# Kernel tuning notes

Hardware: AMD Instinct MI355X
Metric: run time of the kernel (lower is better)

The kernel has to match this reference:

```python
import jax, jax.numpy as jnp
import numpy as np

B, N, C, H = 16, 1024, 768, 12
D = C // H          # head dim = 64
HID = 4 * C         # 3072
EPS = 1e-5


def layernorm(x, g, b):
    m = x.mean(-1, keepdims=True)
    v = ((x - m) ** 2).mean(-1, keepdims=True)
    return (x - m) * jax.lax.rsqrt(v + EPS) * g + b


def setup_inputs() -> dict:
    key = jax.random.key(0)
    ks = jax.random.split(key, 10)
    s = 0.02
    return {
        "x": jax.random.normal(ks[0], (B, N, C), dtype=jnp.float32),
        "ln1_g": jnp.ones((C,), jnp.float32), "ln1_b": jnp.zeros((C,), jnp.float32),
        "wq": jax.random.normal(ks[1], (C, C)) * s, "bq": jnp.zeros((C,), jnp.float32),
        "wk": jax.random.normal(ks[2], (C, C)) * s, "bk": jnp.zeros((C,), jnp.float32),
        "wv": jax.random.normal(ks[3], (C, C)) * s, "bv": jnp.zeros((C,), jnp.float32),
        "wp": jax.random.normal(ks[4], (C, C)) * s, "bp": jnp.zeros((C,), jnp.float32),
        "ln2_g": jnp.ones((C,), jnp.float32), "ln2_b": jnp.zeros((C,), jnp.float32),
        "w1": jax.random.normal(ks[5], (HID, C)) * s, "b1": jnp.zeros((HID,), jnp.float32),
        "w2": jax.random.normal(ks[6], (C, HID)) * s, "b2": jnp.zeros((C,), jnp.float32),
        "gate_h": jax.random.normal(ks[7], (H,), dtype=jnp.float32),
        "gate_f": jax.random.normal(ks[8], (HID,), dtype=jnp.float32),
    }


def reference(x, ln1_g, ln1_b, wq, bq, wk, bk, wv, bv, wp, bp,
              ln2_g, ln2_b, w1, b1, w2, b2, gate_h, gate_f):
    # steady-state path: k_dynamic=None, is_warmup=False -> dyn gates are all ones,
    # so head_mask / ffn_mask reduce to the hard static gates (STE is identity on ones).
    head_mask = (jax.nn.sigmoid(gate_h) > 0.5).astype(x.dtype)            # [H]
    hm = jnp.broadcast_to(head_mask, (B, H))                              # [B,H]

    # --- attention branch ---
    xn = layernorm(x, ln1_g, ln1_b)
    split = lambda t: t.reshape(B, N, H, D).transpose(0, 2, 1, 3)          # [B,H,N,D]
    q = split(xn @ wq.T + bq)
    k = split(xn @ wk.T + bk)
    v = split(xn @ wv.T + bv)
    scale = D ** -0.5
    attn = jax.nn.softmax(jnp.einsum('bhqd,bhkd->bhqk', q, k) * scale, axis=-1)
    y = jnp.einsum('bhqk,bhkd->bhqd', attn, v)
    y = y * hm[:, :, None, None]                                           # per-head mask on y
    xa = y.transpose(0, 2, 1, 3).reshape(B, N, C)
    hm_flat = jnp.repeat(hm, D, axis=-1).reshape(B, 1, C)                  # mask applied a 2nd time
    xa = (xa * hm_flat) @ wp.T + bp
    x = x + xa

    # --- gated MLP branch ---
    fmask = (jax.nn.sigmoid(gate_f) > 0.5).astype(x.dtype)[None, None, :]  # [1,1,HID]
    xn2 = layernorm(x, ln2_g, ln2_b)
    f1 = xn2 @ w1.T + b1
    f1 = jax.nn.gelu(f1 * fmask, approximate=False) * fmask                # mask -> GELU -> mask
    x = x + f1 @ w2.T + b2
    return x
```

## Files before the change

kernel.cpp:

```cpp
#include <hip/hip_runtime.h>

#define BB 16
#define NNN 1024
#define CC 768
#define HH 12
#define DD 64
#define HIDN 3072
#define ROWS (BB*NNN)

typedef _Float16 half8 __attribute__((ext_vector_type(8)));
typedef _Float16 half4 __attribute__((ext_vector_type(4)));
typedef float floatx4 __attribute__((ext_vector_type(4)));

#define GLOAD_LDS(g, l) __builtin_amdgcn_global_load_lds( \
    (const __attribute__((address_space(1))) void*)(g),    \
    (__attribute__((address_space(3))) void*)(l), 16, 0, 0)

#define RAW_BARRIER() do { asm volatile("" ::: "memory"); \
    __builtin_amdgcn_s_barrier(); asm volatile("" ::: "memory"); } while (0)
#define VMCNT_WAIT(n) __builtin_amdgcn_s_waitcnt((n) | 0x0F70)

__global__ void cvt_kernel(const float* __restrict__ src, _Float16* __restrict__ dst, int n4) {
    int i = blockIdx.x * blockDim.x + threadIdx.x;
    if (i < n4) {
        floatx4 v = ((const floatx4*)src)[i];
        half4 h;
        h[0] = (_Float16)v[0]; h[1] = (_Float16)v[1];
        h[2] = (_Float16)v[2]; h[3] = (_Float16)v[3];
        ((half4*)dst)[i] = h;
    }
}

__global__ __launch_bounds__(256) void scan_kernel(const float* __restrict__ gf,
                                                   const float* __restrict__ b1,
                                                   int* __restrict__ meta,
                                                   int* __restrict__ perm,
                                                   float* __restrict__ b1c) {
    int t = threadIdx.x;
    int base = t * 12;
    bool act[12];
    int cnt = 0;
    #pragma unroll
    for (int i = 0; i < 12; i++) { bool a = gf[base + i] > 0.0f; act[i] = a; cnt += a ? 1 : 0; }
    __shared__ int cs[256];
    cs[t] = cnt;
    __syncthreads();
    if (t == 0) {
        int s = 0;
        for (int i = 0; i < 256; i++) { int c = cs[i]; cs[i] = s; s += c; }
        meta[1] = s;
        meta[0] = (s + 127) & ~127;
    }
    __syncthreads();
    int off = cs[t];
    for (int i = t; i < HIDN; i += 256) { b1c[i] = 0.0f; perm[i] = -1; }
    __syncthreads();
    #pragma unroll
    for (int i = 0; i < 12; i++)
        if (act[i]) { perm[off] = base + i; b1c[off] = b1[base + i]; off++; }
}

__global__ void gatherW1_kernel(const float* __restrict__ src, const int* __restrict__ perm,
                                _Float16* __restrict__ dst) {
    int i = blockIdx.x * blockDim.x + threadIdx.x;
    int row = i / 192, c4 = i - row * 192;
    int s = perm[row];
    half4 h; h[0] = h[1] = h[2] = h[3] = (_Float16)0.0f;
    if (s >= 0) {
        floatx4 v = ((const floatx4*)(src + (size_t)s * CC))[c4];
        h[0] = (_Float16)v[0]; h[1] = (_Float16)v[1];
        h[2] = (_Float16)v[2]; h[3] = (_Float16)v[3];
    }
    ((half4*)dst)[i] = h;
}

__global__ void gatherW2_kernel(const float* __restrict__ src, const int* __restrict__ perm,
                                _Float16* __restrict__ dst) {
    int i = blockIdx.x * blockDim.x + threadIdx.x;
    int n = i / 768, j4 = (i - n * 768) * 4;
    const float* r = src + (size_t)n * HIDN;
    half4 h;
    #pragma unroll
    for (int e = 0; e < 4; e++) {
        int s = perm[j4 + e];
        h[e] = (s >= 0) ? (_Float16)r[s] : (_Float16)0.0f;
    }
    *(half4*)&dst[(size_t)n * HIDN + j4] = h;
}

__global__ __launch_bounds__(256) void ln_kernel(const float* __restrict__ x,
                                                 const float* __restrict__ g,
                                                 const float* __restrict__ b,
                                                 _Float16* __restrict__ out) {
    int row = blockIdx.x;
    int t = threadIdx.x;
    const float* xr = x + (size_t)row * CC;
    float v0 = xr[t], v1 = xr[t + 256], v2 = xr[t + 512];
    float s = v0 + v1 + v2;
    float q = v0 * v0 + v1 * v1 + v2 * v2;
    #pragma unroll
    for (int m = 1; m < 64; m <<= 1) {
        s += __shfl_xor(s, m, 64);
        q += __shfl_xor(q, m, 64);
    }
    __shared__ float red[8];
    int wv = t >> 6, lane = t & 63;
    if (lane == 0) { red[wv] = s; red[wv + 4] = q; }
    __syncthreads();
    s = red[0] + red[1] + red[2] + red[3];
    q = red[4] + red[5] + red[6] + red[7];
    float mean = s * (1.0f / CC);
    float var = q * (1.0f / CC) - mean * mean;
    float rs = rsqrtf(var + 1e-5f);
    _Float16* orow = out + (size_t)row * CC;
    orow[t]       = (_Float16)((v0 - mean) * rs * g[t]       + b[t]);
    orow[t + 256] = (_Float16)((v1 - mean) * rs * g[t + 256] + b[t + 256]);
    orow[t + 512] = (_Float16)((v2 - mean) * rs * g[t + 512] + b[t + 512]);
}

template <int MODE>
__global__ __launch_bounds__(256) void gemm_kernel(
    const _Float16* __restrict__ A,
    const _Float16* __restrict__ W,
    const float* __restrict__ bias0,
    const float* __restrict__ bias1,
    const float* __restrict__ bias2,
    const float* __restrict__ res,
    const float* __restrict__ gate,
    const float* __restrict__ hgate,
    void* __restrict__ out0,
    void* __restrict__ out1,
    void* __restrict__ out2,
    const int* __restrict__ meta,
    int M, int N, int K)
{
    int GN = N >> 7, GM = M >> 7;
    int f = blockIdx.x;
    int xcd = f & 7, slot = f >> 3;
    int m_idx = xcd * (GM >> 3) + slot / GN;
    int n_idx = slot - (slot / GN) * GN;
    int m0 = m_idx * 128, n0 = n_idx * 128;

    int Klen = K;
    if (meta) {
        if (MODE == 1) { if (n0 >= meta[0]) return; }
        if (MODE == 2) Klen = meta[0];
    }

    int seg = 0;
    if (MODE == 0) {
        seg = n0 / 768;
        int segc0 = n0 - seg * 768;
        int h0 = segc0 >> 6;
        if (hgate[h0] <= 0.0f && hgate[h0 + 1] <= 0.0f) return;
    }
    unsigned kmask = 0xFFFFFFFFu;
    if (MODE == 2 && hgate) {
        kmask = 0;
        for (int i = 0; i < HH; i++) kmask |= (hgate[i] > 0.0f ? 1u : 0u) << i;
    }

    __shared__ _Float16 As[2][128 * 32];
    __shared__ _Float16 Bs[2][128 * 32];
    int t = threadIdx.x;
    int lane = t & 63, w = t >> 6;
    int wm = (w >> 1) * 64, wn = (w & 1) * 64;
    int L = lane & 15, quad = lane >> 4;
    int rchunk = (quad ^ ((L >> 2) & 3)) * 8;

    floatx4 acc[4][4];
    #pragma unroll
    for (int i = 0; i < 4; i++)
        #pragma unroll
        for (int j = 0; j < 4; j++)
            acc[i][j] = (floatx4){0.f, 0.f, 0.f, 0.f};

    const _Float16* agp[2];
    const _Float16* bgp[2];
    #pragma unroll
    for (int i = 0; i < 2; i++) {
        int pc = i * 256 + t;
        int row = pc >> 2;
        int kc = (pc & 3) ^ ((pc >> 4) & 3);
        agp[i] = A + (size_t)(m0 + row) * K + kc * 8;
        bgp[i] = W + (size_t)(n0 + row) * K + kc * 8;
    }
    unsigned wb = (unsigned)w * 512;

    auto nextk = [&](int k0) -> int {
        if (MODE == 2)
            while (k0 < Klen && !((kmask >> ((k0 >> 6) & 31)) & 1)) k0 += 32;
        return k0;
    };
    auto stage = [&](int buf, int k0) {
        #pragma unroll
        for (int i = 0; i < 2; i++) GLOAD_LDS(agp[i] + k0, &As[buf][i * 2048 + wb]);
        #pragma unroll
        for (int i = 0; i < 2; i++) GLOAD_LDS(bgp[i] + k0, &Bs[buf][i * 2048 + wb]);
    };
    auto compute = [&](int buf) {
        half8 af[4], bf[4];
        #pragma unroll
        for (int i = 0; i < 4; i++) af[i] = *(const half8*)&As[buf][(wm + i * 16 + L) * 32 + rchunk];
        #pragma unroll
        for (int j = 0; j < 4; j++)  bf[j] = *(const half8*)&Bs[buf][(wn + j * 16 + L) * 32 + rchunk];
        #pragma unroll
        for (int i = 0; i < 4; i++)
            #pragma unroll
            for (int j = 0; j < 4; j++)
                acc[i][j] = __builtin_amdgcn_mfma_f32_16x16x32_f16(af[i], bf[j], acc[i][j], 0, 0, 0);
    };

    int kcur = nextk(0);
    if (kcur < Klen) {
        stage(0, kcur);
        int kn1 = nextk(kcur + 32);
        int kn2 = Klen;
        if (kn1 < Klen) { stage(1, kn1); kn2 = nextk(kn1 + 32); }
        int buf = 0;
        while (kn2 < Klen) {
            VMCNT_WAIT(4);
            RAW_BARRIER();
            compute(buf);
            RAW_BARRIER();
            stage(buf, kn2);
            buf ^= 1;
            kn1 = kn2; kn2 = nextk(kn2 + 32);
        }
        if (kn1 < Klen) {
            VMCNT_WAIT(4);
            RAW_BARRIER();
            compute(buf);
            buf ^= 1;
        }
        VMCNT_WAIT(0);
        RAW_BARRIER();
        compute(buf);
    }

    #pragma unroll
    for (int i = 0; i < 4; i++) {
        #pragma unroll
        for (int j = 0; j < 4; j++) {
            int gn = n0 + wn + j * 16 + L;
            if (MODE == 0) {
                int col = gn - seg * 768;
                const float* bsel = (seg == 0) ? bias0 : (seg == 1) ? bias1 : bias2;
                float bs = bsel[col];
                if (seg < 2) {
                    _Float16* o = (_Float16*)((seg == 0) ? out0 : out1);
                    #pragma unroll
                    for (int r = 0; r < 4; r++) {
                        int gm = m0 + wm + i * 16 + quad * 4 + r;
                        o[(size_t)gm * CC + col] = (_Float16)(acc[i][j][r] + bs);
                    }
                } else {
                    int gm0 = m0 + wm + i * 16 + quad * 4;
                    int b_ = gm0 >> 10, n_ = gm0 & 1023;
                    half4 pk;
                    #pragma unroll
                    for (int r = 0; r < 4; r++) pk[r] = (_Float16)(acc[i][j][r] + bs);
                    size_t idx = ((size_t)(b_ * HH + (col >> 6)) * 64 + (col & 63)) * NNN + n_;
                    *(half4*)&((_Float16*)out2)[idx] = pk;
                }
            } else {
                float bs = bias0[gn];
                #pragma unroll
                for (int r = 0; r < 4; r++) {
                    int gm = m0 + wm + i * 16 + quad * 4 + r;
                    float v = acc[i][j][r] + bs;
                    size_t idx = (size_t)gm * N + gn;
                    if (MODE == 1) {
                        float vv = 0.5f * v * (1.0f + erff(v * 0.70710678118f));
                        if (gate && !(gate[gn] > 0.0f)) vv = 0.0f;
                        ((_Float16*)out0)[idx] = (_Float16)vv;
                    } else {
                        ((float*)out0)[idx] = res[idx] + v;
                    }
                }
            }
        }
    }
}

__global__ __launch_bounds__(256) void attn_kernel(
    const _Float16* __restrict__ Q,
    const _Float16* __restrict__ Kp,
    const _Float16* __restrict__ Vt,
    const float* __restrict__ gate_h,
    _Float16* __restrict__ Y)
{
    int qt = blockIdx.x;
    int h  = blockIdx.y;
    int b  = blockIdx.z;
    int t = threadIdx.x;
    int q0 = qt * 64;
    size_t ybase = ((size_t)b * NNN + q0) * CC + h * DD;

    if (gate_h[h] <= 0.0f) {
        int r = t >> 2, c = (t & 3) * 16;
        half8 z = {(_Float16)0, (_Float16)0, (_Float16)0, (_Float16)0,
                   (_Float16)0, (_Float16)0, (_Float16)0, (_Float16)0};
        *(half8*)&Y[ybase + (size_t)r * CC + c]     = z;
        *(half8*)&Y[ybase + (size_t)r * CC + c + 8] = z;
        return;
    }

    __shared__ _Float16 Qs[64][72];
    __shared__ _Float16 Ks[64][72];
    __shared__ _Float16 Vs[64][72];
    __shared__ _Float16 Ps[64][72];

    int lane = t & 63, w = t >> 6;
    int L = lane & 15, quad = lane >> 4;

    {
        int r = t >> 2, c = (t & 3) * 16;
        const half8* src = (const half8*)(Q + ((size_t)b * NNN + q0 + r) * CC + h * DD + c);
        half8 h0 = src[0], h1 = src[1];
        #pragma unroll
        for (int e = 0; e < 8; e++) { h0[e] = h0[e] * (_Float16)0.125f; h1[e] = h1[e] * (_Float16)0.125f; }
        *(half8*)&Qs[r][c]     = h0;
        *(half8*)&Qs[r][c + 8] = h1;
    }

    floatx4 O[4];
    float m_[4], l_[4];
    #pragma unroll
    for (int i = 0; i < 4; i++) { O[i] = (floatx4){0.f,0.f,0.f,0.f}; m_[i] = -1e30f; l_[i] = 0.0f; }

    const size_t kbase = (size_t)b * NNN * CC + h * DD;
    const size_t vbase = (size_t)(b * HH + h) * DD * NNN;

    for (int kt = 0; kt < 16; ++kt) {
        int k0 = kt * 64;
        __syncthreads();
        {
            int r = t >> 2, c = (t & 3) * 16;
            const half8* ks = (const half8*)(Kp + kbase + (size_t)(k0 + r) * CC + c);
            half8 ka = ks[0], kb = ks[1];
            *(half8*)&Ks[r][c]     = ka;
            *(half8*)&Ks[r][c + 8] = kb;
            const half8* vs = (const half8*)(Vt + vbase + (size_t)r * NNN + k0 + c);
            half8 va = vs[0], vb = vs[1];
            *(half8*)&Vs[r][c]     = va;
            *(half8*)&Vs[r][c + 8] = vb;
        }
        __syncthreads();

        half8 aq0 = *(const half8*)&Qs[16 * w + L][quad * 8];
        half8 aq1 = *(const half8*)&Qs[16 * w + L][quad * 8 + 32];
        floatx4 s[4];
        #pragma unroll
        for (int j = 0; j < 4; j++) {
            half8 b0 = *(const half8*)&Ks[16 * j + L][quad * 8];
            half8 b1 = *(const half8*)&Ks[16 * j + L][quad * 8 + 32];
            floatx4 z = (floatx4){0.f,0.f,0.f,0.f};
            z = __builtin_amdgcn_mfma_f32_16x16x32_f16(aq0, b0, z, 0, 0, 0);
            z = __builtin_amdgcn_mfma_f32_16x16x32_f16(aq1, b1, z, 0, 0, 0);
            s[j] = z;
        }

        #pragma unroll
        for (int r = 0; r < 4; r++) {
            float mx = fmaxf(fmaxf(s[0][r], s[1][r]), fmaxf(s[2][r], s[3][r]));
            mx = fmaxf(mx, __shfl_xor(mx, 1, 64));
            mx = fmaxf(mx, __shfl_xor(mx, 2, 64));
            mx = fmaxf(mx, __shfl_xor(mx, 4, 64));
            mx = fmaxf(mx, __shfl_xor(mx, 8, 64));
            float mnew = fmaxf(m_[r], mx);
            float alpha = __expf(m_[r] - mnew);
            m_[r] = mnew;
            float ps = 0.0f;
            #pragma unroll
            for (int j = 0; j < 4; j++) {
                float p = __expf(s[j][r] - mnew);
                s[j][r] = p; ps += p;
                Ps[16 * w + quad * 4 + r][L + 16 * j] = (_Float16)p;
            }
            ps += __shfl_xor(ps, 1, 64);
            ps += __shfl_xor(ps, 2, 64);
            ps += __shfl_xor(ps, 4, 64);
            ps += __shfl_xor(ps, 8, 64);
            l_[r] = l_[r] * alpha + ps;
            #pragma unroll
            for (int t4 = 0; t4 < 4; t4++) O[t4][r] *= alpha;
        }
        __syncthreads();

        half8 ap0 = *(const half8*)&Ps[16 * w + L][quad * 8];
        half8 ap1 = *(const half8*)&Ps[16 * w + L][quad * 8 + 32];
        #pragma unroll
        for (int t4 = 0; t4 < 4; t4++) {
            half8 b0 = *(const half8*)&Vs[16 * t4 + L][quad * 8];
            half8 b1 = *(const half8*)&Vs[16 * t4 + L][quad * 8 + 32];
            O[t4] = __builtin_amdgcn_mfma_f32_16x16x32_f16(ap0, b0, O[t4], 0, 0, 0);
            O[t4] = __builtin_amdgcn_mfma_f32_16x16x32_f16(ap1, b1, O[t4], 0, 0, 0);
        }
    }

    __syncthreads();
    #pragma unroll
    for (int r = 0; r < 4; r++) {
        float inv = 1.0f / l_[r];
        #pragma unroll
        for (int t4 = 0; t4 < 4; t4++)
            Ps[16 * w + quad * 4 + r][16 * t4 + L] = (_Float16)(O[t4][r] * inv);
    }
    __syncthreads();
    {
        int r = t >> 2, c = (t & 3) * 16;
        half8 o0 = *(const half8*)&Ps[r][c];
        half8 o1 = *(const half8*)&Ps[r][c + 8];
        *(half8*)&Y[ybase + (size_t)r * CC + c]     = o0;
        *(half8*)&Y[ybase + (size_t)r * CC + c + 8] = o1;
    }
}

extern "C" void kernel_launch(void* const* d_in, const int* in_sizes, int n_in,
                              void* d_out, int out_size, void* d_ws, size_t ws_size,
                              hipStream_t stream)
{
    const float* x      = (const float*)d_in[0];
    const float* ln1_g  = (const float*)d_in[1];
    const float* ln1_b  = (const float*)d_in[2];
    const float* wq     = (const float*)d_in[3];
    const float* bq     = (const float*)d_in[4];
    const float* wk     = (const float*)d_in[5];
    const float* bk     = (const float*)d_in[6];
    const float* wv     = (const float*)d_in[7];
    const float* bv     = (const float*)d_in[8];
    const float* wp     = (const float*)d_in[9];
    const float* bp     = (const float*)d_in[10];
    const float* ln2_g  = (const float*)d_in[11];
    const float* ln2_b  = (const float*)d_in[12];
    const float* w1     = (const float*)d_in[13];
    const float* b1     = (const float*)d_in[14];
    const float* w2     = (const float*)d_in[15];
    const float* b2     = (const float*)d_in[16];
    const float* gate_h = (const float*)d_in[17];
    const float* gate_f = (const float*)d_in[18];

    char* ws = (char*)d_ws;
    _Float16* WQKVh = (_Float16*)(ws + 0);
    _Float16* WPh = (_Float16*)(ws + 3538944);
    _Float16* W1c = (_Float16*)(ws + 4718592);
    _Float16* W2c = (_Float16*)(ws + 9437184);
    _Float16* XN  = (_Float16*)(ws + 14155776);
    _Float16* Qb  = (_Float16*)(ws + 39321600);
    _Float16* Kb  = (_Float16*)(ws + 64487424);
    _Float16* Vtb = (_Float16*)(ws + 89653248);
    _Float16* Yb  = (_Float16*)(ws + 114819072);
    float*    X1  = (float*)   (ws + 139984896);
    _Float16* XN2 = (_Float16*)(ws + 114819072);
    _Float16* F1  = (_Float16*)(ws + 14155776);
    int*      meta = (int*)    (ws + 190316544);
    int*      perm = (int*)    (ws + 190316800);
    float*    b1c  = (float*)  (ws + 190329088);

    scan_kernel<<<1, 256, 0, stream>>>(gate_f, b1, meta, perm, b1c);

    cvt_kernel<<<576, 256, 0, stream>>>(wq, WQKVh, 147456);
    cvt_kernel<<<576, 256, 0, stream>>>(wk, WQKVh + 589824, 147456);
    cvt_kernel<<<576, 256, 0, stream>>>(wv, WQKVh + 1179648, 147456);
    cvt_kernel<<<576, 256, 0, stream>>>(wp, WPh, 147456);
    gatherW1_kernel<<<2304, 256, 0, stream>>>(w1, perm, W1c);
    gatherW2_kernel<<<2304, 256, 0, stream>>>(w2, perm, W2c);

    ln_kernel<<<ROWS, 256, 0, stream>>>(x, ln1_g, ln1_b, XN);

    gemm_kernel<0><<<2304, 256, 0, stream>>>(
        XN, WQKVh, bq, bk, bv, nullptr, nullptr, gate_h, Qb, Kb, Vtb, nullptr, ROWS, 2304, CC);

    attn_kernel<<<dim3(16, HH, BB), 256, 0, stream>>>(Qb, Kb, Vtb, gate_h, Yb);

    gemm_kernel<2><<<768, 256, 0, stream>>>(
        Yb, WPh, bp, nullptr, nullptr, x, nullptr, gate_h, X1, nullptr, nullptr, nullptr, ROWS, CC, CC);

    ln_kernel<<<ROWS, 256, 0, stream>>>(X1, ln2_g, ln2_b, XN2);

    gemm_kernel<1><<<3072, 256, 0, stream>>>(
        XN2, W1c, b1c, nullptr, nullptr, nullptr, nullptr, nullptr, F1, nullptr, nullptr, meta, ROWS, HIDN, CC);

    gemm_kernel<2><<<768, 256, 0, stream>>>(
        F1, W2c, b2, nullptr, nullptr, X1, nullptr, nullptr, (float*)d_out, nullptr, nullptr, meta, ROWS, CC, HIDN);
}
```

Baseline: 487.7 us.

## Compact QKV weights to active heads and use direct-load GEMM mainloop

A new scan kernel builds a list of active heads, and the QKV weights are gathered into a compacted matrix covering only those heads (padded to an even count). The QKV GEMM and the attention grid then exit early for tiles beyond the active-head width, and the GEMM epilogue remaps compacted columns back to original head positions. This removes the work for masked heads. Separately, the GEMM mainloop no longer stages tiles through LDS with async double buffering. Each wave now loads its MFMA fragments straight from global memory, which gives up data sharing through LDS across waves and relies on cache hits, and this affects every GEMM, including the large MLP ones.

```diff
diff --git a/kernel.cpp b/kernel.cpp
--- a/kernel.cpp
+++ b/kernel.cpp
@@ -12,13 +12,7 @@
 typedef _Float16 half4 __attribute__((ext_vector_type(4)));
 typedef float floatx4 __attribute__((ext_vector_type(4)));
 
-#define GLOAD_LDS(g, l) __builtin_amdgcn_global_load_lds( \
-    (const __attribute__((address_space(1))) void*)(g),    \
-    (__attribute__((address_space(3))) void*)(l), 16, 0, 0)
-
-#define RAW_BARRIER() do { asm volatile("" ::: "memory"); \
-    __builtin_amdgcn_s_barrier(); asm volatile("" ::: "memory"); } while (0)
-#define VMCNT_WAIT(n) __builtin_amdgcn_s_waitcnt((n) | 0x0F70)
+#define MFMA16(acc_, a_, b_) acc_ = __builtin_amdgcn_mfma_f32_16x16x32_f16(a_, b_, acc_, 0, 0, 0)
 
 __global__ void cvt_kernel(const float* __restrict__ src, _Float16* __restrict__ dst, int n4) {
     int i = blockIdx.x * blockDim.x + threadIdx.x;
@@ -29,6 +23,39 @@
         h[2] = (_Float16)v[2]; h[3] = (_Float16)v[3];
         ((half4*)dst)[i] = h;
     }
+}
+
+__global__ void scanh_kernel(const float* __restrict__ gh, int* __restrict__ hmeta,
+                             int* __restrict__ hperm) {
+    if (threadIdx.x == 0 && blockIdx.x == 0) {
+        int c = 0;
+        for (int i = 0; i < HH; i++) if (gh[i] > 0.0f) hperm[c++] = i;
+        for (int i = c; i < HH; i++) hperm[i] = -1;
+        int Hp = (c + 1) & ~1;
+        hmeta[1] = c;
+        hmeta[2] = Hp * 64;
+        hmeta[0] = 3 * Hp * 64;
+    }
+}
+
+__global__ void gatherQKV_kernel(const float* __restrict__ wq, const float* __restrict__ wk,
+                                 const float* __restrict__ wv, const int* __restrict__ hmeta,
+                                 const int* __restrict__ hperm, _Float16* __restrict__ dst) {
+    int i = blockIdx.x * blockDim.x + threadIdx.x;
+    int row = i / 192, c4 = i - row * 192;
+    if (row >= hmeta[0]) return;
+    int segw = hmeta[2];
+    int seg = row / segw, rem = row - seg * segw;
+    int ho = hperm[rem >> 6];
+    half4 h; h[0] = h[1] = h[2] = h[3] = (_Float16)0.0f;
+    if (ho >= 0) {
+        const float* src = (seg == 0 ? wq : seg == 1 ? wk : wv) +
+                           (size_t)(ho * 64 + (rem & 63)) * CC;
+        floatx4 v = ((const floatx4*)src)[c4];
+        h[0] = (_Float16)v[0]; h[1] = (_Float16)v[1];
+        h[2] = (_Float16)v[2]; h[3] = (_Float16)v[3];
+    }
+    ((half4*)&dst[(size_t)row * CC])[c4] = h;
 }
 
 __global__ __launch_bounds__(256) void scan_kernel(const float* __restrict__ gf,
@@ -132,6 +159,7 @@
     void* __restrict__ out1,
     void* __restrict__ out2,
     const int* __restrict__ meta,
+    const int* __restrict__ hperm,
     int M, int N, int K)
 {
     int GN = N >> 7, GM = M >> 7;
@@ -142,31 +170,20 @@
     int m0 = m_idx * 128, n0 = n_idx * 128;
 
     int Klen = K;
-    if (meta) {
-        if (MODE == 1) { if (n0 >= meta[0]) return; }
-        if (MODE == 2) Klen = meta[0];
-    }
-
-    int seg = 0;
-    if (MODE == 0) {
-        seg = n0 / 768;
-        int segc0 = n0 - seg * 768;
-        int h0 = segc0 >> 6;
-        if (hgate[h0] <= 0.0f && hgate[h0 + 1] <= 0.0f) return;
-    }
+    if (MODE == 0) { if (n0 >= meta[0]) return; }
+    if (MODE == 1) { if (n0 >= meta[0]) return; }
+    if (MODE == 2 && meta) Klen = meta[0];
+
     unsigned kmask = 0xFFFFFFFFu;
     if (MODE == 2 && hgate) {
         kmask = 0;
         for (int i = 0; i < HH; i++) kmask |= (hgate[i] > 0.0f ? 1u : 0u) << i;
     }
 
-    __shared__ _Float16 As[2][128 * 32];
-    __shared__ _Float16 Bs[2][128 * 32];
     int t = threadIdx.x;
     int lane = t & 63, w = t >> 6;
     int wm = (w >> 1) * 64, wn = (w & 1) * 64;
     int L = lane & 15, quad = lane >> 4;
-    int rchunk = (quad ^ ((L >> 2) & 3)) * 8;
 
     floatx4 acc[4][4];
     #pragma unroll
@@ -175,84 +192,56 @@
         for (int j = 0; j < 4; j++)
             acc[i][j] = (floatx4){0.f, 0.f, 0.f, 0.f};
 
-    const _Float16* agp[2];
-    const _Float16* bgp[2];
-    #pragma unroll
-    for (int i = 0; i < 2; i++) {
-        int pc = i * 256 + t;
-        int row = pc >> 2;
-        int kc = (pc & 3) ^ ((pc >> 4) & 3);
-        agp[i] = A + (size_t)(m0 + row) * K + kc * 8;
-        bgp[i] = W + (size_t)(n0 + row) * K + kc * 8;
-    }
-    unsigned wb = (unsigned)w * 512;
-
-    auto nextk = [&](int k0) -> int {
-        if (MODE == 2)
-            while (k0 < Klen && !((kmask >> ((k0 >> 6) & 31)) & 1)) k0 += 32;
-        return k0;
-    };
-    auto stage = [&](int buf, int k0) {
-        #pragma unroll
-        for (int i = 0; i < 2; i++) GLOAD_LDS(agp[i] + k0, &As[buf][i * 2048 + wb]);
-        #pragma unroll
-        for (int i = 0; i < 2; i++) GLOAD_LDS(bgp[i] + k0, &Bs[buf][i * 2048 + wb]);
-    };
-    auto compute = [&](int buf) {
+    const _Float16* ap[4];
+    const _Float16* bp[4];
+    #pragma unroll
+    for (int i = 0; i < 4; i++) ap[i] = A + (size_t)(m0 + wm + i * 16 + L) * K + quad * 8;
+    #pragma unroll
+    for (int j = 0; j < 4; j++) bp[j] = W + (size_t)(n0 + wn + j * 16 + L) * K + quad * 8;
+
+    auto step = [&](int k) {
         half8 af[4], bf[4];
         #pragma unroll
-        for (int i = 0; i < 4; i++) af[i] = *(const half8*)&As[buf][(wm + i * 16 + L) * 32 + rchunk];
-        #pragma unroll
-        for (int j = 0; j < 4; j++)  bf[j] = *(const half8*)&Bs[buf][(wn + j * 16 + L) * 32 + rchunk];
+        for (int i = 0; i < 4; i++) af[i] = *(const half8*)(ap[i] + k);
+        #pragma unroll
+        for (int j = 0; j < 4; j++) bf[j] = *(const half8*)(bp[j] + k);
         #pragma unroll
         for (int i = 0; i < 4; i++)
             #pragma unroll
             for (int j = 0; j < 4; j++)
-                acc[i][j] = __builtin_amdgcn_mfma_f32_16x16x32_f16(af[i], bf[j], acc[i][j], 0, 0, 0);
+                MFMA16(acc[i][j], af[i], bf[j]);
     };
 
-    int kcur = nextk(0);
-    if (kcur < Klen) {
-        stage(0, kcur);
-        int kn1 = nextk(kcur + 32);
-        int kn2 = Klen;
-        if (kn1 < Klen) { stage(1, kn1); kn2 = nextk(kn1 + 32); }
-        int buf = 0;
-        while (kn2 < Klen) {
-            VMCNT_WAIT(4);
-            RAW_BARRIER();
-            compute(buf);
-            RAW_BARRIER();
-            stage(buf, kn2);
-            buf ^= 1;
-            kn1 = kn2; kn2 = nextk(kn2 + 32);
-        }
-        if (kn1 < Klen) {
-            VMCNT_WAIT(4);
-            RAW_BARRIER();
-            compute(buf);
-            buf ^= 1;
-        }
-        VMCNT_WAIT(0);
-        RAW_BARRIER();
-        compute(buf);
-    }
-
-    #pragma unroll
-    for (int i = 0; i < 4; i++) {
-        #pragma unroll
-        for (int j = 0; j < 4; j++) {
-            int gn = n0 + wn + j * 16 + L;
-            if (MODE == 0) {
-                int col = gn - seg * 768;
+    if (MODE == 2 && hgate) {
+        for (int k = 0; k < Klen; k += 32) {
+            if (!((kmask >> ((k >> 6) & 31)) & 1)) continue;
+            step(k);
+        }
+    } else {
+        #pragma unroll 2
+        for (int k = 0; k < Klen; k += 32) step(k);
+    }
+
+    if (MODE == 0) {
+        int segw = meta[2];
+        int seg = n0 / segw;
+        int cbase = n0 - seg * segw + wn;
+        int ho = hperm[cbase >> 6];
+        if (ho < 0) return;
+        #pragma unroll
+        for (int i = 0; i < 4; i++) {
+            #pragma unroll
+            for (int j = 0; j < 4; j++) {
+                int d = j * 16 + L;
+                int ocol = ho * 64 + d;
                 const float* bsel = (seg == 0) ? bias0 : (seg == 1) ? bias1 : bias2;
-                float bs = bsel[col];
+                float bs = bsel[ocol];
                 if (seg < 2) {
                     _Float16* o = (_Float16*)((seg == 0) ? out0 : out1);
                     #pragma unroll
                     for (int r = 0; r < 4; r++) {
                         int gm = m0 + wm + i * 16 + quad * 4 + r;
-                        o[(size_t)gm * CC + col] = (_Float16)(acc[i][j][r] + bs);
+                        o[(size_t)gm * CC + ocol] = (_Float16)(acc[i][j][r] + bs);
                     }
                 } else {
                     int gm0 = m0 + wm + i * 16 + quad * 4;
@@ -260,10 +249,17 @@
                     half4 pk;
                     #pragma unroll
                     for (int r = 0; r < 4; r++) pk[r] = (_Float16)(acc[i][j][r] + bs);
-                    size_t idx = ((size_t)(b_ * HH + (col >> 6)) * 64 + (col & 63)) * NNN + n_;
+                    size_t idx = ((size_t)(b_ * HH + ho) * 64 + d) * NNN + n_;
                     *(half4*)&((_Float16*)out2)[idx] = pk;
                 }
-            } else {
+            }
+        }
+    } else {
+        #pragma unroll
+        for (int i = 0; i < 4; i++) {
+            #pragma unroll
+            for (int j = 0; j < 4; j++) {
+                int gn = n0 + wn + j * 16 + L;
                 float bs = bias0[gn];
                 #pragma unroll
                 for (int r = 0; r < 4; r++) {
@@ -287,24 +283,18 @@
     const _Float16* __restrict__ Q,
     const _Float16* __restrict__ Kp,
     const _Float16* __restrict__ Vt,
-    const float* __restrict__ gate_h,
+    const int* __restrict__ hmeta,
+    const int* __restrict__ hperm,
     _Float16* __restrict__ Y)
 {
     int qt = blockIdx.x;
-    int h  = blockIdx.y;
+    int hc = blockIdx.y;
     int b  = blockIdx.z;
+    if (hc >= hmeta[1]) return;
+    int h = hperm[hc];
     int t = threadIdx.x;
     int q0 = qt * 64;
     size_t ybase = ((size_t)b * NNN + q0) * CC + h * DD;
-
-    if (gate_h[h] <= 0.0f) {
-        int r = t >> 2, c = (t & 3) * 16;
-        half8 z = {(_Float16)0, (_Float16)0, (_Float16)0, (_Float16)0,
-                   (_Float16)0, (_Float16)0, (_Float16)0, (_Float16)0};
-        *(half8*)&Y[ybase + (size_t)r * CC + c]     = z;
-        *(half8*)&Y[ybase + (size_t)r * CC + c + 8] = z;
-        return;
-    }
 
     __shared__ _Float16 Qs[64][72];
     __shared__ _Float16 Ks[64][72];
@@ -442,7 +432,7 @@
     const float* gate_f = (const float*)d_in[18];
 
     char* ws = (char*)d_ws;
-    _Float16* WQKVh = (_Float16*)(ws + 0);
+    _Float16* WQKVc = (_Float16*)(ws + 0);
     _Float16* WPh = (_Float16*)(ws + 3538944);
     _Float16* W1c = (_Float16*)(ws + 4718592);
     _Float16* W2c = (_Float16*)(ws + 9437184);
@@ -457,12 +447,13 @@
     int*      meta = (int*)    (ws + 190316544);
     int*      perm = (int*)    (ws + 190316800);
     float*    b1c  = (float*)  (ws + 190329088);
+    int*      hmeta = (int*)   (ws + 190341376);
+    int*      hperm = (int*)   (ws + 190341440);
 
     scan_kernel<<<1, 256, 0, stream>>>(gate_f, b1, meta, perm, b1c);
-
-    cvt_kernel<<<576, 256, 0, stream>>>(wq, WQKVh, 147456);
-    cvt_kernel<<<576, 256, 0, stream>>>(wk, WQKVh + 589824, 147456);
-    cvt_kernel<<<576, 256, 0, stream>>>(wv, WQKVh + 1179648, 147456);
+    scanh_kernel<<<1, 64, 0, stream>>>(gate_h, hmeta, hperm);
+
+    gatherQKV_kernel<<<1728, 256, 0, stream>>>(wq, wk, wv, hmeta, hperm, WQKVc);
     cvt_kernel<<<576, 256, 0, stream>>>(wp, WPh, 147456);
     gatherW1_kernel<<<2304, 256, 0, stream>>>(w1, perm, W1c);
     gatherW2_kernel<<<2304, 256, 0, stream>>>(w2, perm, W2c);
@@ -470,18 +461,18 @@
     ln_kernel<<<ROWS, 256, 0, stream>>>(x, ln1_g, ln1_b, XN);
 
     gemm_kernel<0><<<2304, 256, 0, stream>>>(
-        XN, WQKVh, bq, bk, bv, nullptr, nullptr, gate_h, Qb, Kb, Vtb, nullptr, ROWS, 2304, CC);
-
-    attn_kernel<<<dim3(16, HH, BB), 256, 0, stream>>>(Qb, Kb, Vtb, gate_h, Yb);
+        XN, WQKVc, bq, bk, bv, nullptr, nullptr, nullptr, Qb, Kb, Vtb, hmeta, hperm, ROWS, 2304, CC);
+
+    attn_kernel<<<dim3(16, HH, BB), 256, 0, stream>>>(Qb, Kb, Vtb, hmeta, hperm, Yb);
 
     gemm_kernel<2><<<768, 256, 0, stream>>>(
-        Yb, WPh, bp, nullptr, nullptr, x, nullptr, gate_h, X1, nullptr, nullptr, nullptr, ROWS, CC, CC);
+        Yb, WPh, bp, nullptr, nullptr, x, nullptr, gate_h, X1, nullptr, nullptr, nullptr, nullptr, ROWS, CC, CC);
 
     ln_kernel<<<ROWS, 256, 0, stream>>>(X1, ln2_g, ln2_b, XN2);
 
     gemm_kernel<1><<<3072, 256, 0, stream>>>(
-        XN2, W1c, b1c, nullptr, nullptr, nullptr, nullptr, nullptr, F1, nullptr, nullptr, meta, ROWS, HIDN, CC);
+        XN2, W1c, b1c, nullptr, nullptr, nullptr, nullptr, nullptr, F1, nullptr, nullptr, meta, nullptr, ROWS, HIDN, CC);
 
     gemm_kernel<2><<<768, 256, 0, stream>>>(
-        F1, W2c, b2, nullptr, nullptr, X1, nullptr, nullptr, (float*)d_out, nullptr, nullptr, meta, ROWS, CC, HIDN);
-}
+        F1, W2c, b2, nullptr, nullptr, X1, nullptr, nullptr, (float*)d_out, nullptr, nullptr, meta, nullptr, ROWS, CC, HIDN);
+}
```

Measured after the change: 697.3 us. +43.0%, slower.
